# Optimization experiments

Measured on AMD Instinct MI355X. Metric: run time of the kernel, lower is better.

## Reference

```python
import jax, jax.numpy as jnp
import numpy as np

N_NODES = 50000
N_EDGES = 600000
IN_DIM = 128
HID = 128
N_LAYERS = 4
N_GRAPHS = 128
N_CLASSES = 10
SPARSITY = 0.5
BN_EPS = 1e-5


def setup_inputs() -> dict:
    key = jax.random.key(0)
    ks = jax.random.split(key, 16)
    h = jax.random.normal(ks[0], (N_NODES, IN_DIM), dtype=jnp.float32)
    snorm_n = jax.random.uniform(ks[1], (N_NODES, 1), dtype=jnp.float32)
    src = jax.random.randint(ks[2], (N_EDGES,), 0, N_NODES, dtype=jnp.int32)
    dst = jax.random.randint(ks[3], (N_EDGES,), 0, N_NODES, dtype=jnp.int32)
    graph_ids = jnp.sort(jax.random.randint(ks[4], (N_NODES,), 0, N_GRAPHS, dtype=jnp.int32))
    # Expander (sparsity-masked) linear params
    embed_W = 0.1 * jax.random.normal(ks[5], (HID, IN_DIM), dtype=jnp.float32)
    embed_mask = (jax.random.uniform(ks[6], (HID, IN_DIM)) < SPARSITY).astype(jnp.float32)
    embed_b = jnp.zeros((HID,), dtype=jnp.float32)
    layer_W = 0.1 * jax.random.normal(ks[7], (N_LAYERS, HID, HID), dtype=jnp.float32)
    layer_mask = (jax.random.uniform(ks[8], (N_LAYERS, HID, HID)) < SPARSITY).astype(jnp.float32)
    layer_b = jnp.zeros((N_LAYERS, HID), dtype=jnp.float32)
    gamma = jnp.ones((N_LAYERS, HID), dtype=jnp.float32)
    beta = jnp.zeros((N_LAYERS, HID), dtype=jnp.float32)
    ro_W = 0.1 * jax.random.normal(ks[9], (N_CLASSES, HID), dtype=jnp.float32)
    ro_b = jnp.zeros((N_CLASSES,), dtype=jnp.float32)
    return {"h": h, "snorm_n": snorm_n, "src": src, "dst": dst, "graph_ids": graph_ids,
            "embed_W": embed_W, "embed_mask": embed_mask, "embed_b": embed_b,
            "layer_W": layer_W, "layer_mask": layer_mask, "layer_b": layer_b,
            "gamma": gamma, "beta": beta, "ro_W": ro_W, "ro_b": ro_b}


def reference(h, snorm_n, src, dst, graph_ids, embed_W, embed_mask, embed_b,
              layer_W, layer_mask, layer_b, gamma, beta, ro_W, ro_b):
    n = h.shape[0]
    # embedding_h: sparsity-masked linear
    h = h @ (embed_W * embed_mask).T + embed_b
    for l in range(layer_W.shape[0]):
        h_in = h
        # message passing: copy_src + sum reduce over edges
        agg = jax.ops.segment_sum(h[src], dst, num_segments=n)  # [N, HID]
        # node apply: masked linear MLP (n_mlp=1)
        z = agg @ (layer_W[l] * layer_mask[l]).T + layer_b[l]
        # graph norm
        z = z * snorm_n
        # batch norm (training-mode batch statistics)
        mu = jnp.mean(z, axis=0)
        var = jnp.var(z, axis=0)
        z = (z - mu) * jax.lax.rsqrt(var + BN_EPS) * gamma[l] + beta[l]
        # activation + residual
        z = jax.nn.relu(z)
        h = h_in + z
    # mean readout over graphs (segment mean)
    sums = jax.ops.segment_sum(h, graph_ids, num_segments=N_GRAPHS)  # [G, HID]
    cnt = jax.ops.segment_sum(jnp.ones((n, 1), h.dtype), graph_ids, num_segments=N_GRAPHS)
    hg = sums / jnp.maximum(cnt, 1.0)
    return hg @ ro_W.T + ro_b
```

## Files before the change

kernel.cpp:

```cpp
#include <hip/hip_runtime.h>
#include <hip/hip_bf16.h>

#define N_NODES   50000
#define N_EDGES   600000
#define HID       128
#define N_LAYERS  4
#define N_GRAPHS  128
#define N_CLASSES 10
#define BN_EPS    1e-5f

#define RSPLIT 8
#define GEMM_GRID ((N_NODES + 63) / 64)
#define CVT_N   3200000
#define CVT_GRID ((CVT_N + 255) / 256)
#define NREP 32
#define ELL_W 64

#define OFF_WMT   0u
#define OFF_H     81920u
#define OFF_Z     (OFF_H + 6400000u)
#define OFF_H0BF  (OFF_Z + 6400000u)
#define OFF_ZERO  (OFF_H0BF + 3200000u)
#define OFF_CSUMR OFF_ZERO
#define OFF_SUMS  (OFF_CSUMR + 32768u)
#define OFF_DEG   (OFF_SUMS + 16384u)
#define ZERO_N    (32768u + 16384u + 50000u)
#define OFF_ELL   (OFF_ZERO + ZERO_N)
#define OFF_GST   (OFF_ELL + 3200000u)
#define OFF_CSUMF (OFF_GST + 132u)
#define OFF_HBF   (OFF_CSUMF + 1024u)

#define PRE_ZB 388
#define PRE_WB 160
#define PRE_BB 196

typedef __attribute__((ext_vector_type(8))) short short8;
typedef __attribute__((ext_vector_type(4))) float f32x4;

__device__ __forceinline__ unsigned int bf16_of(float f) {
    unsigned int u = __float_as_uint(f);
    return (u + 0x7fffu + ((u >> 16) & 1u)) >> 16;
}
__device__ __forceinline__ unsigned int pack_bf2(float lo, float hi) {
    return bf16_of(lo) | (bf16_of(hi) << 16);
}

__global__ __launch_bounds__(256) void preamble_kernel(
    int* __restrict__ zbase,
    const float* __restrict__ We, const float* __restrict__ Me,
    const float* __restrict__ Wl, const float* __restrict__ Ml,
    unsigned int* __restrict__ Wbf,
    const int* __restrict__ gid, int* __restrict__ g_start)
{
    int b = blockIdx.x;
    if (b < PRE_ZB) {
        int i = b * 256 + threadIdx.x;
        if (i < (int)ZERO_N) zbase[i] = 0;
    } else if (b < PRE_ZB + PRE_WB) {
        int i = (b - PRE_ZB) * 256 + threadIdx.x;
        if (i < 5 * 8192) {
            int m = i >> 13;
            int j = i & 8191;
            int c = j >> 6, ku = j & 63;
            const float* Wsrc = (m == 0) ? We : Wl + (m - 1) * 16384;
            const float* Msrc = (m == 0) ? Me : Ml + (m - 1) * 16384;
            int base = c * 128 + ku * 2;
            float w0 = Wsrc[base] * Msrc[base];
            float w1 = Wsrc[base + 1] * Msrc[base + 1];
            unsigned int h0 = bf16_of(w0), h1 = bf16_of(w1);
            float l0 = w0 - __uint_as_float(h0 << 16);
            float l1 = w1 - __uint_as_float(h1 << 16);
            Wbf[m * 16384 + c * 64 + ku]        = h0 | (h1 << 16);
            Wbf[m * 16384 + 8192 + c * 64 + ku] = bf16_of(l0) | (bf16_of(l1) << 16);
        }
    } else {
        int i = (b - PRE_ZB - PRE_WB) * 256 + threadIdx.x;
        if (i >= N_NODES) return;
        int g = gid[i];
        if (i == 0) {
            for (int x = 0; x <= g; ++x) g_start[x] = 0;
        } else {
            int gp = gid[i - 1];
            for (int x = gp + 1; x <= g; ++x) g_start[x] = i;
        }
        if (i == N_NODES - 1) {
            for (int x = g + 1; x <= N_GRAPHS; ++x) g_start[x] = N_NODES;
        }
    }
}

__global__ __launch_bounds__(256) void ellfill_kernel(const int* __restrict__ src,
                                                      const int* __restrict__ dst,
                                                      int* __restrict__ deg,
                                                      int* __restrict__ ell, int nE) {
    int i = blockIdx.x * 256 + threadIdx.x;
    if (i < nE) {
        int d = dst[i];
        int slot = atomicAdd(&deg[d], 1);
        if (slot < ELL_W) ell[(size_t)d * ELL_W + slot] = src[i];
    }
}

__global__ __launch_bounds__(256) void cvt_kernel(const float2* __restrict__ src,
                                                  unsigned int* __restrict__ dst, int n) {
    int i = blockIdx.x * 256 + threadIdx.x;
    if (i < n) {
        float2 v = src[i];
        dst[i] = pack_bf2(v.x, v.y);
    }
}

__global__ __launch_bounds__(256) void gemm_mfma(
    const uint4* __restrict__ Abf,
    const unsigned int* __restrict__ Wmat,
    const float* __restrict__ bias,
    float* __restrict__ Z, unsigned int* __restrict__ hbf, int nRows)
{
    __shared__ unsigned int As[64 * 64];
    int tid = threadIdx.x;
    int w  = tid >> 6;
    int l  = tid & 63;
    int q  = l >> 4;
    int ri = l & 15;
    int r0 = blockIdx.x * 64;

    short8 bfrag[2][2][4];
    const uint4* W4 = (const uint4*)Wmat;
#pragma unroll
    for (int p = 0; p < 2; ++p)
#pragma unroll
        for (int ct2 = 0; ct2 < 2; ++ct2) {
            int c = (w * 2 + ct2) * 16 + ri;
#pragma unroll
            for (int kc = 0; kc < 4; ++kc) {
                uint4 t = W4[p * 2048 + c * 16 + kc * 4 + q];
                bfrag[p][ct2][kc] = *(short8*)&t;
            }
        }

#pragma unroll
    for (int it = 0; it < 4; ++it) {
        int e = tid + it * 256;
        int r = e >> 4, g = e & 15;
        int gr = r0 + r;
        if (gr >= nRows) gr = nRows - 1;
        uint4 v = Abf[(size_t)gr * 16 + g];
        *(uint4*)&As[r * 64 + ((g ^ (r & 7)) << 2)] = v;
    }
    __syncthreads();

    f32x4 zero4 = {0.f, 0.f, 0.f, 0.f};
    f32x4 acc[4][2];
#pragma unroll
    for (int rt = 0; rt < 4; ++rt)
#pragma unroll
        for (int ct2 = 0; ct2 < 2; ++ct2) acc[rt][ct2] = zero4;

#pragma unroll
    for (int kc = 0; kc < 4; ++kc)
#pragma unroll
        for (int rt = 0; rt < 4; ++rt) {
            int row = rt * 16 + ri;
            short8 af = *(const short8*)&As[row * 64 + (((kc * 4 + q) ^ (ri & 7)) << 2)];
#pragma unroll
            for (int ct2 = 0; ct2 < 2; ++ct2) {
                acc[rt][ct2] = __builtin_amdgcn_mfma_f32_16x16x32_bf16(
                    af, bfrag[0][ct2][kc], acc[rt][ct2], 0, 0, 0);
                acc[rt][ct2] = __builtin_amdgcn_mfma_f32_16x16x32_bf16(
                    af, bfrag[1][ct2][kc], acc[rt][ct2], 0, 0, 0);
            }
        }

    unsigned short* hb = (unsigned short*)hbf;
#pragma unroll
    for (int ct2 = 0; ct2 < 2; ++ct2) {
        int col = (w * 2 + ct2) * 16 + ri;
        float bb = bias[col];
#pragma unroll
        for (int rt = 0; rt < 4; ++rt)
#pragma unroll
            for (int reg = 0; reg < 4; ++reg) {
                int row = r0 + rt * 16 + q * 4 + reg;
                if (row < nRows) {
                    float v = acc[rt][ct2][reg] + bb;
                    Z[(size_t)row * 128 + col] = v;
                    hb[(size_t)row * 128 + col] = (unsigned short)bf16_of(v);
                }
            }
    }
}

__global__ __launch_bounds__(256) void agg_gemm_mfma(
    const unsigned int* __restrict__ Hbf,
    const int* __restrict__ deg, const int* __restrict__ ell,
    const unsigned int* __restrict__ Wmat,
    const float* __restrict__ bias, const float* __restrict__ snorm,
    float* __restrict__ Z, float* __restrict__ colsum, int nRows)
{
    __shared__ unsigned int As[64 * 64];
    int tid = threadIdx.x;
    int w  = tid >> 6;
    int l  = tid & 63;
    int q  = l >> 4;
    int ri = l & 15;
    int half = l >> 5;
    int l4   = l & 31;
    int r0 = blockIdx.x * 64;

    const uint2* H2 = (const uint2*)Hbf;
#pragma unroll
    for (int iter = 0; iter < 8; ++iter) {
        int rl = iter * 8 + w * 2 + half;
        int node = r0 + rl;
        if (node >= nRows) node = nRows - 1;
        int dg = deg[node];
        const int* ep = ell + (size_t)node * ELL_W;
        float4 a0 = make_float4(0.f, 0.f, 0.f, 0.f);
        float4 a1 = make_float4(0.f, 0.f, 0.f, 0.f);
        float4 a2 = make_float4(0.f, 0.f, 0.f, 0.f);
        float4 a3 = make_float4(0.f, 0.f, 0.f, 0.f);
#define ACCUM(AX, V)                                                        \
        AX.x += __uint_as_float((V).x << 16);                               \
        AX.y += __uint_as_float((V).x & 0xffff0000u);                       \
        AX.z += __uint_as_float((V).y << 16);                               \
        AX.w += __uint_as_float((V).y & 0xffff0000u);
        int e = 0;
        for (; e + 7 < dg; e += 8) {
            int s0 = ep[e],     s1 = ep[e + 1], s2 = ep[e + 2], s3 = ep[e + 3];
            int s4 = ep[e + 4], s5 = ep[e + 5], s6 = ep[e + 6], s7 = ep[e + 7];
            uint2 v0 = H2[(size_t)s0 * 32 + l4];
            uint2 v1 = H2[(size_t)s1 * 32 + l4];
            uint2 v2 = H2[(size_t)s2 * 32 + l4];
            uint2 v3 = H2[(size_t)s3 * 32 + l4];
            uint2 v4 = H2[(size_t)s4 * 32 + l4];
            uint2 v5 = H2[(size_t)s5 * 32 + l4];
            uint2 v6 = H2[(size_t)s6 * 32 + l4];
            uint2 v7 = H2[(size_t)s7 * 32 + l4];
            ACCUM(a0, v0) ACCUM(a1, v1) ACCUM(a2, v2) ACCUM(a3, v3)
            ACCUM(a0, v4) ACCUM(a1, v5) ACCUM(a2, v6) ACCUM(a3, v7)
        }
        for (; e + 3 < dg; e += 4) {
            int s0 = ep[e], s1 = ep[e + 1], s2 = ep[e + 2], s3 = ep[e + 3];
            uint2 v0 = H2[(size_t)s0 * 32 + l4];
            uint2 v1 = H2[(size_t)s1 * 32 + l4];
            uint2 v2 = H2[(size_t)s2 * 32 + l4];
            uint2 v3 = H2[(size_t)s3 * 32 + l4];
            ACCUM(a0, v0) ACCUM(a1, v1) ACCUM(a2, v2) ACCUM(a3, v3)
        }
        for (; e < dg; ++e) {
            uint2 v0 = H2[(size_t)ep[e] * 32 + l4];
            ACCUM(a0, v0)
        }
#undef ACCUM
        a0.x += a1.x; a0.y += a1.y; a0.z += a1.z; a0.w += a1.w;
        a2.x += a3.x; a2.y += a3.y; a2.z += a3.z; a2.w += a3.w;
        a0.x += a2.x; a0.y += a2.y; a0.z += a2.z; a0.w += a2.w;
        uint2 o;
        o.x = pack_bf2(a0.x, a0.y);
        o.y = pack_bf2(a0.z, a0.w);
        int g16 = l4 >> 1;
        *(uint2*)&As[rl * 64 + ((g16 ^ (rl & 7)) << 2) + (l4 & 1) * 2] = o;
    }

    short8 bfrag[2][2][4];
    const uint4* W4 = (const uint4*)Wmat;
#pragma unroll
    for (int p = 0; p < 2; ++p)
#pragma unroll
        for (int ct2 = 0; ct2 < 2; ++ct2) {
            int c = (w * 2 + ct2) * 16 + ri;
#pragma unroll
            for (int kc = 0; kc < 4; ++kc) {
                uint4 t = W4[p * 2048 + c * 16 + kc * 4 + q];
                bfrag[p][ct2][kc] = *(short8*)&t;
            }
        }
    __syncthreads();

    f32x4 zero4 = {0.f, 0.f, 0.f, 0.f};
    f32x4 acc[4][2];
#pragma unroll
    for (int rt = 0; rt < 4; ++rt)
#pragma unroll
        for (int ct2 = 0; ct2 < 2; ++ct2) acc[rt][ct2] = zero4;

#pragma unroll
    for (int kc = 0; kc < 4; ++kc)
#pragma unroll
        for (int rt = 0; rt < 4; ++rt) {
            int row = rt * 16 + ri;
            short8 af = *(const short8*)&As[row * 64 + (((kc * 4 + q) ^ (ri & 7)) << 2)];
#pragma unroll
            for (int ct2 = 0; ct2 < 2; ++ct2) {
                acc[rt][ct2] = __builtin_amdgcn_mfma_f32_16x16x32_bf16(
                    af, bfrag[0][ct2][kc], acc[rt][ct2], 0, 0, 0);
                acc[rt][ct2] = __builtin_amdgcn_mfma_f32_16x16x32_bf16(
                    af, bfrag[1][ct2][kc], acc[rt][ct2], 0, 0, 0);
            }
        }

    float csv[2] = {0.f, 0.f}, cqv[2] = {0.f, 0.f};
#pragma unroll
    for (int ct2 = 0; ct2 < 2; ++ct2) {
        int col = (w * 2 + ct2) * 16 + ri;
        float bb = bias[col];
#pragma unroll
        for (int rt = 0; rt < 4; ++rt)
#pragma unroll
            for (int reg = 0; reg < 4; ++reg) {
                int row = r0 + rt * 16 + q * 4 + reg;
                if (row < nRows) {
                    float sn = snorm[row];
                    float v = (acc[rt][ct2][reg] + bb) * sn;
                    Z[(size_t)row * 128 + col] = v;
                    csv[ct2] += v;
                    cqv[ct2] += v * v;
                }
            }
    }
    {
        float* cdst = colsum + ((blockIdx.x & (NREP - 1)) << 8);
#pragma unroll
        for (int ct2 = 0; ct2 < 2; ++ct2) {
            float s  = csv[ct2], sq = cqv[ct2];
            s  += __shfl_xor(s, 16);  s  += __shfl_xor(s, 32);
            sq += __shfl_xor(sq, 16); sq += __shfl_xor(sq, 32);
            if (q == 0) {
                int col = (w * 2 + ct2) * 16 + ri;
                atomicAdd(&cdst[col], s);
                atomicAdd(&cdst[128 + col], sq);
            }
        }
    }
}

__global__ __launch_bounds__(256) void bnred_kernel(const float* __restrict__ rep,
                                                    float* __restrict__ outp) {
    int t = threadIdx.x;
    float s = 0.f;
#pragma unroll
    for (int r = 0; r < NREP; ++r) s += rep[r * 256 + t];
    outp[t] = s;
}

__global__ __launch_bounds__(256) void apply_kernel(const float* __restrict__ Z,
                                                    const float* __restrict__ csum,
                                                    const float* __restrict__ gamma,
                                                    const float* __restrict__ beta,
                                                    float* __restrict__ H,
                                                    unsigned int* __restrict__ hbf,
                                                    int n4, int layer) {
    int i = blockIdx.x * 256 + threadIdx.x;
    if (i >= n4) return;
    int c4 = i & 31;
    const float invN = 1.0f / (float)N_NODES;
    float4 s  = ((const float4*)(csum  + layer * 256))[c4];
    float4 q  = ((const float4*)(csum  + layer * 256 + 128))[c4];
    float4 g  = ((const float4*)(gamma + layer * 128))[c4];
    float4 be = ((const float4*)(beta  + layer * 128))[c4];
    float4 z = ((const float4*)Z)[i];
    float4 h = ((float4*)H)[i];
    float mu, var, sc, sh;
    mu = s.x * invN; var = q.x * invN - mu * mu; sc = g.x * rsqrtf(var + BN_EPS); sh = be.x - mu * sc;
    h.x += fmaxf(z.x * sc + sh, 0.f);
    mu = s.y * invN; var = q.y * invN - mu * mu; sc = g.y * rsqrtf(var + BN_EPS); sh = be.y - mu * sc;
    h.y += fmaxf(z.y * sc + sh, 0.f);
    mu = s.z * invN; var = q.z * invN - mu * mu; sc = g.z * rsqrtf(var + BN_EPS); sh = be.z - mu * sc;
    h.z += fmaxf(z.z * sc + sh, 0.f);
    mu = s.w * invN; var = q.w * invN - mu * mu; sc = g.w * rsqrtf(var + BN_EPS); sh = be.w - mu * sc;
    h.w += fmaxf(z.w * sc + sh, 0.f);
    ((float4*)H)[i] = h;
    hbf[i * 2]     = pack_bf2(h.x, h.y);
    hbf[i * 2 + 1] = pack_bf2(h.z, h.w);
}

__global__ __launch_bounds__(256) void readout2_kernel(const float* __restrict__ H,
                                                       const int* __restrict__ g_start,
                                                       float* __restrict__ sums) {
    int g     = blockIdx.x / RSPLIT;
    int chunk = blockIdx.x % RSPLIT;
    int beg = g_start[g], end = g_start[g + 1];
    int col  = threadIdx.x & 127;
    int half = threadIdx.x >> 7;
    float acc = 0.f;
    for (int r = beg + chunk * 2 + half; r < end; r += RSPLIT * 2) {
        acc += H[(size_t)r * 128 + col];
    }
    if (acc != 0.f || half == 0)
        atomicAdd(&sums[g * 128 + col], acc);
}

__global__ __launch_bounds__(128) void final_kernel(const float* __restrict__ sums,
                                                    const int* __restrict__ g_start,
                                                    const float* __restrict__ roW,
                                                    const float* __restrict__ rob,
                                                    float* __restrict__ out) {
    __shared__ float row[128];
    int g = blockIdx.x;
    int t = threadIdx.x;
    float c = fmaxf((float)(g_start[g + 1] - g_start[g]), 1.0f);
    row[t] = sums[g * 128 + t] / c;
    __syncthreads();
    if (t < N_CLASSES) {
        float s = rob[t];
        for (int k = 0; k < 128; ++k) s += row[k] * roW[t * 128 + k];
        out[g * N_CLASSES + t] = s;
    }
}

extern "C" void kernel_launch(void* const* d_in, const int* in_sizes, int n_in,
                              void* d_out, int out_size, void* d_ws, size_t ws_size,
                              hipStream_t stream) {
    const float* h0      = (const float*)d_in[0];
    const float* snorm   = (const float*)d_in[1];
    const int*   src     = (const int*)d_in[2];
    const int*   dst     = (const int*)d_in[3];
    const int*   gid     = (const int*)d_in[4];
    const float* embedW  = (const float*)d_in[5];
    const float* embedM  = (const float*)d_in[6];
    const float* embedB  = (const float*)d_in[7];
    const float* layerW  = (const float*)d_in[8];
    const float* layerM  = (const float*)d_in[9];
    const float* layerB  = (const float*)d_in[10];
    const float* gamma   = (const float*)d_in[11];
    const float* beta    = (const float*)d_in[12];
    const float* roW     = (const float*)d_in[13];
    const float* rob     = (const float*)d_in[14];
    float* out = (float*)d_out;

    float* ws   = (float*)d_ws;
    unsigned int* Wbf = (unsigned int*)(ws + OFF_WMT);
    float* H    = ws + OFF_H;
    float* Z    = ws + OFF_Z;
    unsigned int* h0bf = (unsigned int*)(ws + OFF_H0BF);
    float* csumr = ws + OFF_CSUMR;
    float* csumf = ws + OFF_CSUMF;
    float* sums = ws + OFF_SUMS;
    int*   deg  = (int*)(ws + OFF_DEG);
    int*   ell  = (int*)(ws + OFF_ELL);
    int*   gst  = (int*)(ws + OFF_GST);
    unsigned int* Hbf = (unsigned int*)(ws + OFF_HBF);

    preamble_kernel<<<PRE_ZB + PRE_WB + PRE_BB, 256, 0, stream>>>(
        (int*)(ws + OFF_ZERO), embedW, embedM, layerW, layerM, Wbf, gid, gst);
    ellfill_kernel<<<(N_EDGES + 255) / 256, 256, 0, stream>>>(src, dst, deg, ell, N_EDGES);

    cvt_kernel<<<CVT_GRID, 256, 0, stream>>>((const float2*)h0, h0bf, CVT_N);
    gemm_mfma<<<GEMM_GRID, 256, 0, stream>>>((const uint4*)h0bf, Wbf, embedB,
                                             H, Hbf, N_NODES);

    for (int l = 0; l < N_LAYERS; ++l) {
        agg_gemm_mfma<<<GEMM_GRID, 256, 0, stream>>>(
            Hbf, deg, ell, Wbf + (1 + l) * 16384,
            layerB + l * 128, snorm, Z, csumr + l * (NREP * 256), N_NODES);
        bnred_kernel<<<1, 256, 0, stream>>>(csumr + l * (NREP * 256), csumf + l * 256);
        apply_kernel<<<(N_NODES * HID / 4) / 256, 256, 0, stream>>>(
            Z, csumf, gamma, beta, H, Hbf, N_NODES * HID / 4, l);
    }

    readout2_kernel<<<N_GRAPHS * RSPLIT, 256, 0, stream>>>(H, gst, sums);
    final_kernel<<<N_GRAPHS, 128, 0, stream>>>(sums, gst, roW, rob, out);
}
```

Baseline: 522.7 us.

## Split fused gather-aggregate and GEMM into separate aggregate and GEMM kernels

Un-fuses the per-layer kernel. Neighbor aggregation now runs as its own kernel with one half-wave per node, writing bf16 aggregates to a new workspace buffer, and a plain MFMA GEMM kernel then loads those rows into LDS. The aim is to decouple the latency-bound gather from the GEMM tile, so the gather gets full occupancy and is not serialized over 8 iterations per block. In exchange it adds an extra global write and read of the aggregate buffer, plus one more launch per layer. It also clamps the degree to ELL_W.

```diff
diff --git a/kernel.cpp b/kernel.cpp
--- a/kernel.cpp
+++ b/kernel.cpp
@@ -20,7 +20,8 @@
 #define OFF_H     81920u
 #define OFF_Z     (OFF_H + 6400000u)
 #define OFF_H0BF  (OFF_Z + 6400000u)
-#define OFF_ZERO  (OFF_H0BF + 3200000u)
+#define OFF_AGGBF (OFF_H0BF + 3200000u)
+#define OFF_ZERO  (OFF_AGGBF + 3200000u)
 #define OFF_CSUMR OFF_ZERO
 #define OFF_SUMS  (OFF_CSUMR + 32768u)
 #define OFF_DEG   (OFF_SUMS + 16384u)
@@ -110,7 +111,68 @@
     }
 }
 
-__global__ __launch_bounds__(256) void gemm_mfma(
+__global__ __launch_bounds__(256) void aggregate_kernel(const unsigned int* __restrict__ Hbf,
+                                                        const int* __restrict__ deg,
+                                                        const int* __restrict__ ell,
+                                                        unsigned int* __restrict__ aggbf,
+                                                        int nN) {
+    int wid  = (blockIdx.x * 256 + threadIdx.x) >> 6;
+    int lane = threadIdx.x & 63;
+    int half = lane >> 5;
+    int l4   = lane & 31;
+    int node = wid * 2 + half;
+    if (node >= nN) return;
+    int dg = deg[node];
+    if (dg > ELL_W) dg = ELL_W;
+    const int* ep = ell + (size_t)node * ELL_W;
+    const uint2* H2 = (const uint2*)Hbf;
+    float4 a0 = make_float4(0.f, 0.f, 0.f, 0.f);
+    float4 a1 = make_float4(0.f, 0.f, 0.f, 0.f);
+    float4 a2 = make_float4(0.f, 0.f, 0.f, 0.f);
+    float4 a3 = make_float4(0.f, 0.f, 0.f, 0.f);
+#define ACCUM(AX, V)                                                        \
+    AX.x += __uint_as_float((V).x << 16);                                   \
+    AX.y += __uint_as_float((V).x & 0xffff0000u);                           \
+    AX.z += __uint_as_float((V).y << 16);                                   \
+    AX.w += __uint_as_float((V).y & 0xffff0000u);
+    int e = 0;
+    for (; e + 7 < dg; e += 8) {
+        int s0 = ep[e],     s1 = ep[e + 1], s2 = ep[e + 2], s3 = ep[e + 3];
+        int s4 = ep[e + 4], s5 = ep[e + 5], s6 = ep[e + 6], s7 = ep[e + 7];
+        uint2 v0 = H2[(size_t)s0 * 32 + l4];
+        uint2 v1 = H2[(size_t)s1 * 32 + l4];
+        uint2 v2 = H2[(size_t)s2 * 32 + l4];
+        uint2 v3 = H2[(size_t)s3 * 32 + l4];
+        uint2 v4 = H2[(size_t)s4 * 32 + l4];
+        uint2 v5 = H2[(size_t)s5 * 32 + l4];
+        uint2 v6 = H2[(size_t)s6 * 32 + l4];
+        uint2 v7 = H2[(size_t)s7 * 32 + l4];
+        ACCUM(a0, v0) ACCUM(a1, v1) ACCUM(a2, v2) ACCUM(a3, v3)
+        ACCUM(a0, v4) ACCUM(a1, v5) ACCUM(a2, v6) ACCUM(a3, v7)
+    }
+    for (; e + 3 < dg; e += 4) {
+        int s0 = ep[e], s1 = ep[e + 1], s2 = ep[e + 2], s3 = ep[e + 3];
+        uint2 v0 = H2[(size_t)s0 * 32 + l4];
+        uint2 v1 = H2[(size_t)s1 * 32 + l4];
+        uint2 v2 = H2[(size_t)s2 * 32 + l4];
+        uint2 v3 = H2[(size_t)s3 * 32 + l4];
+        ACCUM(a0, v0) ACCUM(a1, v1) ACCUM(a2, v2) ACCUM(a3, v3)
+    }
+    for (; e < dg; ++e) {
+        uint2 v0 = H2[(size_t)ep[e] * 32 + l4];
+        ACCUM(a0, v0)
+    }
+#undef ACCUM
+    a0.x += a1.x; a0.y += a1.y; a0.z += a1.z; a0.w += a1.w;
+    a2.x += a3.x; a2.y += a3.y; a2.z += a3.z; a2.w += a3.w;
+    a0.x += a2.x; a0.y += a2.y; a0.z += a2.z; a0.w += a2.w;
+    uint2 o;
+    o.x = pack_bf2(a0.x, a0.y);
+    o.y = pack_bf2(a0.z, a0.w);
+    ((uint2*)aggbf)[(size_t)node * 32 + l4] = o;
+}
+
+__global__ __launch_bounds__(256) void gemm_mfma_embed(
     const uint4* __restrict__ Abf,
     const unsigned int* __restrict__ Wmat,
     const float* __restrict__ bias,
@@ -190,9 +252,8 @@
     }
 }
 
-__global__ __launch_bounds__(256) void agg_gemm_mfma(
-    const unsigned int* __restrict__ Hbf,
-    const int* __restrict__ deg, const int* __restrict__ ell,
+__global__ __launch_bounds__(256) void gemm_mfma_layer(
+    const uint4* __restrict__ Abf,
     const unsigned int* __restrict__ Wmat,
     const float* __restrict__ bias, const float* __restrict__ snorm,
     float* __restrict__ Z, float* __restrict__ colsum, int nRows)
@@ -203,64 +264,7 @@
     int l  = tid & 63;
     int q  = l >> 4;
     int ri = l & 15;
-    int half = l >> 5;
-    int l4   = l & 31;
     int r0 = blockIdx.x * 64;
-
-    const uint2* H2 = (const uint2*)Hbf;
-#pragma unroll
-    for (int iter = 0; iter < 8; ++iter) {
-        int rl = iter * 8 + w * 2 + half;
-        int node = r0 + rl;
-        if (node >= nRows) node = nRows - 1;
-        int dg = deg[node];
-        const int* ep = ell + (size_t)node * ELL_W;
-        float4 a0 = make_float4(0.f, 0.f, 0.f, 0.f);
-        float4 a1 = make_float4(0.f, 0.f, 0.f, 0.f);
-        float4 a2 = make_float4(0.f, 0.f, 0.f, 0.f);
-        float4 a3 = make_float4(0.f, 0.f, 0.f, 0.f);
-#define ACCUM(AX, V)                                                        \
-        AX.x += __uint_as_float((V).x << 16);                               \
-        AX.y += __uint_as_float((V).x & 0xffff0000u);                       \
-        AX.z += __uint_as_float((V).y << 16);                               \
-        AX.w += __uint_as_float((V).y & 0xffff0000u);
-        int e = 0;
-        for (; e + 7 < dg; e += 8) {
-            int s0 = ep[e],     s1 = ep[e + 1], s2 = ep[e + 2], s3 = ep[e + 3];
-            int s4 = ep[e + 4], s5 = ep[e + 5], s6 = ep[e + 6], s7 = ep[e + 7];
-            uint2 v0 = H2[(size_t)s0 * 32 + l4];
-            uint2 v1 = H2[(size_t)s1 * 32 + l4];
-            uint2 v2 = H2[(size_t)s2 * 32 + l4];
-            uint2 v3 = H2[(size_t)s3 * 32 + l4];
-            uint2 v4 = H2[(size_t)s4 * 32 + l4];
-            uint2 v5 = H2[(size_t)s5 * 32 + l4];
-            uint2 v6 = H2[(size_t)s6 * 32 + l4];
-            uint2 v7 = H2[(size_t)s7 * 32 + l4];
-            ACCUM(a0, v0) ACCUM(a1, v1) ACCUM(a2, v2) ACCUM(a3, v3)
-            ACCUM(a0, v4) ACCUM(a1, v5) ACCUM(a2, v6) ACCUM(a3, v7)
-        }
-        for (; e + 3 < dg; e += 4) {
-            int s0 = ep[e], s1 = ep[e + 1], s2 = ep[e + 2], s3 = ep[e + 3];
-            uint2 v0 = H2[(size_t)s0 * 32 + l4];
-            uint2 v1 = H2[(size_t)s1 * 32 + l4];
-            uint2 v2 = H2[(size_t)s2 * 32 + l4];
-            uint2 v3 = H2[(size_t)s3 * 32 + l4];
-            ACCUM(a0, v0) ACCUM(a1, v1) ACCUM(a2, v2) ACCUM(a3, v3)
-        }
-        for (; e < dg; ++e) {
-            uint2 v0 = H2[(size_t)ep[e] * 32 + l4];
-            ACCUM(a0, v0)
-        }
-#undef ACCUM
-        a0.x += a1.x; a0.y += a1.y; a0.z += a1.z; a0.w += a1.w;
-        a2.x += a3.x; a2.y += a3.y; a2.z += a3.z; a2.w += a3.w;
-        a0.x += a2.x; a0.y += a2.y; a0.z += a2.z; a0.w += a2.w;
-        uint2 o;
-        o.x = pack_bf2(a0.x, a0.y);
-        o.y = pack_bf2(a0.z, a0.w);
-        int g16 = l4 >> 1;
-        *(uint2*)&As[rl * 64 + ((g16 ^ (rl & 7)) << 2) + (l4 & 1) * 2] = o;
-    }
 
     short8 bfrag[2][2][4];
     const uint4* W4 = (const uint4*)Wmat;
@@ -275,6 +279,16 @@
                 bfrag[p][ct2][kc] = *(short8*)&t;
             }
         }
+
+#pragma unroll
+    for (int it = 0; it < 4; ++it) {
+        int e = tid + it * 256;
+        int r = e >> 4, g = e & 15;
+        int gr = r0 + r;
+        if (gr >= nRows) gr = nRows - 1;
+        uint4 v = Abf[(size_t)gr * 16 + g];
+        *(uint4*)&As[r * 64 + ((g ^ (r & 7)) << 2)] = v;
+    }
     __syncthreads();
 
     f32x4 zero4 = {0.f, 0.f, 0.f, 0.f};
@@ -432,7 +446,8 @@
     unsigned int* Wbf = (unsigned int*)(ws + OFF_WMT);
     float* H    = ws + OFF_H;
     float* Z    = ws + OFF_Z;
-    unsigned int* h0bf = (unsigned int*)(ws + OFF_H0BF);
+    unsigned int* h0bf  = (unsigned int*)(ws + OFF_H0BF);
+    unsigned int* aggbf = (unsigned int*)(ws + OFF_AGGBF);
     float* csumr = ws + OFF_CSUMR;
     float* csumf = ws + OFF_CSUMF;
     float* sums = ws + OFF_SUMS;
@@ -446,13 +461,16 @@
     ellfill_kernel<<<(N_EDGES + 255) / 256, 256, 0, stream>>>(src, dst, deg, ell, N_EDGES);
 
     cvt_kernel<<<CVT_GRID, 256, 0, stream>>>((const float2*)h0, h0bf, CVT_N);
-    gemm_mfma<<<GEMM_GRID, 256, 0, stream>>>((const uint4*)h0bf, Wbf, embedB,
-                                             H, Hbf, N_NODES);
-
+    gemm_mfma_embed<<<GEMM_GRID, 256, 0, stream>>>((const uint4*)h0bf, Wbf, embedB,
+                                                   H, Hbf, N_NODES);
+
+    const int agg_grid = (N_NODES / 2 + 3) / 4;
     for (int l = 0; l < N_LAYERS; ++l) {
-        agg_gemm_mfma<<<GEMM_GRID, 256, 0, stream>>>(
-            Hbf, deg, ell, Wbf + (1 + l) * 16384,
-            layerB + l * 128, snorm, Z, csumr + l * (NREP * 256), N_NODES);
+        aggregate_kernel<<<agg_grid, 256, 0, stream>>>(Hbf, deg, ell, aggbf, N_NODES);
+        gemm_mfma_layer<<<GEMM_GRID, 256, 0, stream>>>((const uint4*)aggbf,
+                                                       Wbf + (1 + l) * 16384,
+                                                       layerB + l * 128, snorm,
+                                                       Z, csumr + l * (NREP * 256), N_NODES);
         bnred_kernel<<<1, 256, 0, stream>>>(csumr + l * (NREP * 256), csumf + l * 256);
         apply_kernel<<<(N_NODES * HID / 4) / 256, 256, 0, stream>>>(
             Z, csumf, gamma, beta, H, Hbf, N_NODES * HID / 4, l);
```

After: 442.9 us. 15.3% less time.
